# Kernel tuning notes

Measured on AMD Instinct MI355X. Metric: run time of the kernel, lower is better.

Reference implementation:

```python
import jax, jax.numpy as jnp
import numpy as np
import math

B, S, D, H = 2, 2048, 4096, 32
HD = D // H  # 128


def setup_inputs() -> dict:
    key = jax.random.key(0)
    ks = jax.random.split(key, 8)
    x = jax.random.normal(ks[0], (B, S, D), dtype=jnp.float32)
    wq = jax.random.normal(ks[1], (D, D), dtype=jnp.float32) * 0.02
    wk = jax.random.normal(ks[2], (D, D), dtype=jnp.float32) * 0.02
    wv = jax.random.normal(ks[3], (D, D), dtype=jnp.float32) * 0.02
    wo = jax.random.normal(ks[4], (D, D), dtype=jnp.float32) * 0.02
    # RoPE frequencies as in LLaMA: theta = 10000^{-2i/hd}
    inv_freq = 1.0 / (10000.0 ** (np.arange(0, HD, 2, dtype=np.float32) / HD))  # [HD/2]
    t = np.arange(S, dtype=np.float32)
    freqs = np.outer(t, inv_freq)  # [S, HD/2]
    freqs_cos = jnp.asarray(np.cos(freqs))
    freqs_sin = jnp.asarray(np.sin(freqs))
    # additive causal mask [1,1,S,S]
    neg = jnp.full((S, S), -1e9, dtype=jnp.float32)
    mask = jnp.triu(neg, k=1)[None, None, :, :]
    return {"x": x, "wq": wq, "wk": wk, "wv": wv, "wo": wo,
            "freqs_cos": freqs_cos, "freqs_sin": freqs_sin, "mask": mask}


def _apply_rope(t, cos, sin):
    # t: [b, s, h, hd]; cos/sin: [s, hd/2]. Complex mult on (even, odd) pairs.
    tr = t.reshape(*t.shape[:-1], HD // 2, 2)
    xr, xi = tr[..., 0], tr[..., 1]
    c = cos[None, :, None, :]
    s = sin[None, :, None, :]
    out_r = xr * c - xi * s
    out_i = xr * s + xi * c
    return jnp.stack([out_r, out_i], axis=-1).reshape(t.shape)


def reference(x, wq, wk, wv, wo, freqs_cos, freqs_sin, mask):
    b, s, d = x.shape
    # projections (nn.Linear: y = x @ W^T)
    xq = (x @ wq.T).reshape(b, s, H, HD)
    xk = (x @ wk.T).reshape(b, s, H, HD)
    xv = (x @ wv.T).reshape(b, s, H, HD)
    xq = _apply_rope(xq, freqs_cos, freqs_sin)
    xk = _apply_rope(xk, freqs_cos, freqs_sin)
    # [b,h,q,k] scores, softmax in fp32, then attend
    scores = jnp.einsum('bqhd,bkhd->bhqk', xq, xk) / math.sqrt(HD)
    scores = scores + mask
    probs = jax.nn.softmax(scores.astype(jnp.float32), axis=-1).astype(xq.dtype)
    out = jnp.einsum('bhqk,bkhd->bqhd', probs, xv).reshape(b, s, d)
    return out @ wo.T
```

## Files before the change

### kernel.cpp

```cpp
#include <hip/hip_runtime.h>

typedef __bf16 bf16x8 __attribute__((ext_vector_type(8)));
typedef float f32x4 __attribute__((ext_vector_type(4)));
typedef float f32x16 __attribute__((ext_vector_type(16)));
typedef unsigned short u16;
typedef unsigned int u32;
typedef u16 u16x8 __attribute__((ext_vector_type(8)));
typedef u16 u16x4 __attribute__((ext_vector_type(4)));
typedef u32 u32x4 __attribute__((ext_vector_type(4)));

#define B_ 2
#define S_ 2048
#define D_ 4096
#define H_ 32
#define HD_ 128
#define SM_SCALE 0.08838834764831845f
#define C2_ 0.12751743f

__device__ __forceinline__ u16 f2bf(float f) {
  __bf16 h = (__bf16)f;
  return __builtin_bit_cast(unsigned short, h);
}
__device__ __forceinline__ float bf2f(u16 u) {
  return (float)__builtin_bit_cast(__bf16, u);
}

#define GLD_TO_LDS16(gsrc, ldst)                                                     \
  __builtin_amdgcn_global_load_lds((__attribute__((address_space(1))) void*)(gsrc),  \
                                   (__attribute__((address_space(3))) void*)(ldst),  \
                                   16, 0, 0)

__global__ __launch_bounds__(256) void cvt_kernel(const float* __restrict__ src,
                                                  u16* __restrict__ dst, int n4) {
  int i = blockIdx.x * blockDim.x + threadIdx.x;
  int stride = gridDim.x * blockDim.x;
  for (; i < n4; i += stride) {
    float4 v = reinterpret_cast<const float4*>(src)[i];
    u16x4 o;
    o[0] = f2bf(v.x); o[1] = f2bf(v.y); o[2] = f2bf(v.z); o[3] = f2bf(v.w);
    reinterpret_cast<u16x4*>(dst)[i] = o;
  }
}

__global__ __launch_bounds__(256) void rope_kernel(u16* __restrict__ T,
                                                   const float* __restrict__ fc,
                                                   const float* __restrict__ fs) {
  const int n = B_ * S_ * D_ / 2;
  int i = blockIdx.x * blockDim.x + threadIdx.x;
  int stride = gridDim.x * blockDim.x;
  unsigned int* Tp = reinterpret_cast<unsigned int*>(T);
  for (; i < n; i += stride) {
    int row = i >> 11;
    int pr = i & 2047;
    int s = row & (S_ - 1);
    int p = pr & 63;
    float c = fc[(s << 6) + p];
    float sn = fs[(s << 6) + p];
    unsigned int u = Tp[i];
    float xr = bf2f((u16)(u & 0xffff));
    float xi = bf2f((u16)(u >> 16));
    float orr = xr * c - xi * sn;
    float oii = xr * sn + xi * c;
    Tp[i] = (unsigned int)f2bf(orr) | ((unsigned int)f2bf(oii) << 16);
  }
}


#define LGKM0()                                            \
  do {                                                     \
    asm volatile("s_waitcnt lgkmcnt(0)" ::: "memory");     \
    __builtin_amdgcn_sched_barrier(0);                     \
  } while (0)

__device__ __forceinline__ void fill_af(bf16x8 (&dst)[4], const u16* half_base,
                                        int wr, int lane, int ks) {
#pragma unroll
  for (int m = 0; m < 4; ++m) {
    int rr = wr * 64 + m * 16 + (lane & 15);
    int c8 = (ks * 4 + (lane >> 4)) ^ (rr & 7);
    dst[m] = *reinterpret_cast<const bf16x8*>(half_base + rr * 64 + c8 * 8);
  }
}
__device__ __forceinline__ void fill_bf(bf16x8 (&dst)[2][2], const u16* half_base,
                                        int wn, int lane) {
#pragma unroll
  for (int ks = 0; ks < 2; ++ks)
#pragma unroll
    for (int n = 0; n < 2; ++n) {
      int rr = wn * 32 + n * 16 + (lane & 15);
      int c8 = (ks * 4 + (lane >> 4)) ^ (rr & 7);
      dst[ks][n] = *reinterpret_cast<const bf16x8*>(half_base + rr * 64 + c8 * 8);
    }
}

#define MFMA8(MQ, NQ, KS, AF, BF)                                                \
  do {                                                                           \
    __builtin_amdgcn_s_setprio(1);                                               \
    _Pragma("unroll") for (int m = 0; m < 4; ++m)                                \
      _Pragma("unroll") for (int n = 0; n < 2; ++n)                              \
        acc[(MQ) * 4 + m][(NQ) * 2 + n] =                                        \
            __builtin_amdgcn_mfma_f32_16x16x32_bf16(                             \
                (AF)[m], (BF)[KS][n], acc[(MQ) * 4 + m][(NQ) * 2 + n], 0, 0, 0); \
    __builtin_amdgcn_s_setprio(0);                                               \
  } while (0)

template <typename OutT>
__global__ __launch_bounds__(512, 2) void gemm256_kernel(const u16* __restrict__ A,
                                                         const u16* __restrict__ Bw,
                                                         OutT* __restrict__ C,
                                                         int M, int N, int K) {
  __shared__ u16 As[2][2][8192];
  __shared__ u16 Bs[2][2][8192];
  const int tid = threadIdx.x;
  const int lane = tid & 63;
  const int w = tid >> 6;
  const int wr = w >> 2;
  const int wn = w & 3;
  const int nbx = N >> 8;
  const int nby = M >> 8;
  const int nwg = nby * nbx;
  int tr, tc;
  if (nby == 16 && nbx == 16) {
    int xcd = blockIdx.x & 7, j = blockIdx.x >> 3;
    tr = (xcd >> 1) * 4 + (j >> 3);
    tc = (xcd & 1) * 8 + (j & 7);
  } else {
    int wg = blockIdx.x;
    if ((nwg & 7) == 0) wg = (wg & 7) * (nwg >> 3) + (wg >> 3);
    tr = wg / nbx; tc = wg % nbx;
  }

  const size_t arow0 = (size_t)tr * 256;
  const size_t brow0 = (size_t)tc * 256;
  const int KT = K >> 6;

  auto stageA = [&](int t, int half) {
    if (t >= KT) return;
    const int k0 = t << 6;
    u16* base = &As[t & 1][half][0];
#pragma unroll
    for (int i = 0; i < 2; ++i) {
      int q = i * 512 + tid;
      int r = q >> 3;
      int c8 = (q & 7) ^ (r & 7);
      GLD_TO_LDS16(A + (arow0 + half * 128 + r) * K + k0 + c8 * 8, base + q * 8);
    }
  };
  auto stageB = [&](int t, int half) {
    if (t >= KT) return;
    const int k0 = t << 6;
    u16* base = &Bs[t & 1][half][0];
#pragma unroll
    for (int i = 0; i < 2; ++i) {
      int q = i * 512 + tid;
      int r = q >> 3;
      int c8 = (q & 7) ^ (r & 7);
      GLD_TO_LDS16(Bw + (brow0 + half * 128 + r) * K + k0 + c8 * 8, base + q * 8);
    }
  };

  f32x4 acc[8][4] = {};
  bf16x8 afX[4], afY[4], bf0[2][2], bf1[2][2];

  stageA(0, 0); stageA(0, 1); stageB(0, 0); stageB(0, 1);
  stageB(1, 0); stageB(1, 1); stageA(1, 1);
  asm volatile("s_waitcnt vmcnt(4)" ::: "memory");
  __builtin_amdgcn_s_barrier();
  __builtin_amdgcn_sched_barrier(0);
  fill_af(afX, &As[0][0][0], wr, lane, 0);
  fill_bf(bf0, &Bs[0][0][0], wn, lane);

  for (int k = 0; k < KT; ++k) {
    const int buf = k & 1, nb = buf ^ 1;
    const u16* A0 = &As[buf][0][0];
    const u16* A1 = &As[buf][1][0];
    const u16* B1L = &Bs[buf][1][0];
    const u16* A0n = &As[nb][0][0];
    const u16* B0n = &Bs[nb][0][0];

    LGKM0();
    fill_af(afY, A0, wr, lane, 1);
    fill_bf(bf1, B1L, wn, lane);
    stageA(k + 1, 0);
    MFMA8(0, 0, 0, afX, bf0);
    LGKM0();
    fill_af(afX, A1, wr, lane, 0);
    MFMA8(0, 0, 1, afY, bf0);
    __builtin_amdgcn_s_barrier();

    LGKM0();
    fill_af(afY, A1, wr, lane, 1);
    stageB(k + 2, 0);
    MFMA8(1, 0, 0, afX, bf0);
    LGKM0();
    fill_af(afX, A1, wr, lane, 0);
    MFMA8(1, 0, 1, afY, bf0);
    __builtin_amdgcn_s_barrier();

    LGKM0();
    fill_af(afY, A1, wr, lane, 1);
    stageB(k + 2, 1);
    MFMA8(1, 1, 0, afX, bf1);
    LGKM0();
    fill_af(afX, A0, wr, lane, 0);
    MFMA8(1, 1, 1, afY, bf1);
    __builtin_amdgcn_s_barrier();

    LGKM0();
    fill_af(afY, A0, wr, lane, 1);
    MFMA8(0, 1, 0, afX, bf1);
    LGKM0();
    stageA(k + 2, 1);
    if (k >= KT - 3) asm volatile("s_waitcnt vmcnt(0)" ::: "memory");
    else             asm volatile("s_waitcnt vmcnt(4)" ::: "memory");
    __builtin_amdgcn_s_barrier();
    __builtin_amdgcn_sched_barrier(0);
    if (k + 1 < KT) {
      fill_af(afX, A0n, wr, lane, 0);
      fill_bf(bf0, B0n, wn, lane);
    }
    MFMA8(0, 1, 1, afY, bf1);
    __builtin_amdgcn_s_barrier();
  }

#pragma unroll
  for (int mi = 0; mi < 8; ++mi) {
    const int mq = mi >> 2, m = mi & 3;
#pragma unroll
    for (int ni = 0; ni < 4; ++ni) {
      const int nq = ni >> 1, n = ni & 1;
#pragma unroll
      for (int r = 0; r < 4; ++r) {
        size_t row = arow0 + mq * 128 + wr * 64 + m * 16 + ((lane >> 4) << 2) + r;
        size_t col = (size_t)tc * 256 + nq * 128 + wn * 32 + n * 16 + (lane & 15);
        float v = acc[mi][ni][r];
        if constexpr (__is_same(OutT, float)) {
          C[row * N + col] = v;
        } else {
          C[row * N + col] = f2bf(v);
        }
      }
    }
  }
}

__global__ __launch_bounds__(256, 2) void attn_kernel(const u16* __restrict__ Q,
                                                      const u16* __restrict__ K,
                                                      const u16* __restrict__ V,
                                                      u16* __restrict__ O) {
  __shared__ u16 Ks[2][64 * 128];
  __shared__ u16 Vt[2][128 * 64];

  const int blk = blockIdx.x;
  const int qt = 15 - (blk >> 6);
  const int bh = blk & 63;
  const int b = bh >> 5, h = bh & 31;
  const int q0 = qt << 7;
  const int tid = threadIdx.x, lane = tid & 63, w = tid >> 6;
  const int wq0 = q0 + w * 32;
  const int l31 = lane & 31;
  const int hi = lane >> 5;
  const int qg = wq0 + l31;

  bf16x8 qf[8];
#pragma unroll
  for (int kb = 0; kb < 8; ++kb)
    qf[kb] = *reinterpret_cast<const bf16x8*>(Q + (size_t)(b * S_ + qg) * D_ + h * HD_ + kb * 16 + hi * 8);

  f32x16 oacc[4] = {};
  float mrun = -__builtin_inff(), lrun = 0.f;

  const int ntiles = 2 * qt + 2;
  u16x8 vreg[4];

  {
#pragma unroll
    for (int it = 0; it < 4; ++it) {
      int ff = it * 256 + tid;
      int row = ff >> 4, cc = ff & 15;
      int scc = cc ^ (row & 7);
      GLD_TO_LDS16(K + (size_t)(b * S_ + row) * D_ + h * HD_ + scc * 8, &Ks[0][ff << 3]);
    }
#pragma unroll
    for (int it = 0; it < 4; ++it) {
      int ff = it * 256 + tid;
      int r = ff & 63, dc = ff >> 6;
      vreg[it] = *reinterpret_cast<const u16x8*>(V + (size_t)(b * S_ + r) * D_ + h * HD_ + dc * 8);
    }
#pragma unroll
    for (int it = 0; it < 4; ++it) {
      int ff = it * 256 + tid;
      int r = ff & 63, dc = ff >> 6;
#pragma unroll
      for (int j = 0; j < 8; ++j) {
        int d = dc * 8 + j;
        Vt[0][(d << 6) + (((r >> 3) ^ (d & 7)) << 3) + (r & 7)] = vreg[it][j];
      }
    }
  }
  __syncthreads();

  for (int t = 0; t < ntiles; ++t) {
    const int cur = t & 1, nxt = cur ^ 1;
    const bool pre = (t + 1 < ntiles);
    if (pre) {
      const int kv1 = (t + 1) << 6;
#pragma unroll
      for (int it = 0; it < 4; ++it) {
        int ff = it * 256 + tid;
        int row = ff >> 4, cc = ff & 15;
        int scc = cc ^ (row & 7);
        GLD_TO_LDS16(K + (size_t)(b * S_ + kv1 + row) * D_ + h * HD_ + scc * 8, &Ks[nxt][ff << 3]);
      }
#pragma unroll
      for (int it = 0; it < 4; ++it) {
        int ff = it * 256 + tid;
        int r = ff & 63, dc = ff >> 6;
        vreg[it] = *reinterpret_cast<const u16x8*>(V + (size_t)(b * S_ + kv1 + r) * D_ + h * HD_ + dc * 8);
      }
    }

    const int kv0 = t << 6;
    if (kv0 <= wq0 + 31) {
      f32x16 st[2] = {};
      __builtin_amdgcn_s_setprio(1);
#pragma unroll
      for (int kvh = 0; kvh < 2; ++kvh) {
#pragma unroll
        for (int kb = 0; kb < 8; ++kb) {
          int row = kvh * 32 + l31;
          int cc = (2 * kb + hi) ^ (row & 7);
          bf16x8 kf = *reinterpret_cast<const bf16x8*>(&Ks[cur][(row << 7) + (cc << 3)]);
          st[kvh] = __builtin_amdgcn_mfma_f32_32x32x16_bf16(kf, qf[kb], st[kvh], 0, 0, 0);
        }
      }
      __builtin_amdgcn_s_setprio(0);

      if (kv0 + 63 > wq0) {
#pragma unroll
        for (int kvh = 0; kvh < 2; ++kvh)
#pragma unroll
          for (int r = 0; r < 16; ++r) {
            int kvg = kv0 + kvh * 32 + (r & 3) + 8 * (r >> 2) + 4 * hi;
            if (kvg > qg) st[kvh][r] = -1e30f;
          }
      }

      float vmax = -1e30f;
#pragma unroll
      for (int kvh = 0; kvh < 2; ++kvh)
#pragma unroll
        for (int r = 0; r < 16; ++r) vmax = fmaxf(vmax, st[kvh][r]);
      vmax = fmaxf(vmax, __shfl_xor(vmax, 32));
      float mnew = fmaxf(mrun, vmax);
      float sc = exp2f((mrun - mnew) * C2_);
      mrun = mnew;
      float psum = 0.f;
#pragma unroll
      for (int kvh = 0; kvh < 2; ++kvh)
#pragma unroll
        for (int r = 0; r < 16; ++r) {
          float p = exp2f((st[kvh][r] - mnew) * C2_);
          st[kvh][r] = p;
          psum += p;
        }
      psum += __shfl_xor(psum, 32);
      lrun = lrun * sc + psum;
#pragma unroll
      for (int db = 0; db < 4; ++db)
#pragma unroll
        for (int r = 0; r < 16; ++r) oacc[db][r] *= sc;

      __builtin_amdgcn_s_setprio(1);
#pragma unroll
      for (int h2 = 0; h2 < 2; ++h2)
#pragma unroll
        for (int s2 = 0; s2 < 2; ++s2) {
          const int rb = s2 * 8;
          u32 w0, w1, w2, w3;
          asm("v_cvt_pk_bf16_f32 %0, %1, %2" : "=v"(w0) : "v"(st[h2][rb + 0]), "v"(st[h2][rb + 1]));
          asm("v_cvt_pk_bf16_f32 %0, %1, %2" : "=v"(w1) : "v"(st[h2][rb + 2]), "v"(st[h2][rb + 3]));
          asm("v_cvt_pk_bf16_f32 %0, %1, %2" : "=v"(w2) : "v"(st[h2][rb + 4]), "v"(st[h2][rb + 5]));
          asm("v_cvt_pk_bf16_f32 %0, %1, %2" : "=v"(w3) : "v"(st[h2][rb + 6]), "v"(st[h2][rb + 7]));
          u32 sw0 = (u32)__shfl_xor((int)w0, 32);
          u32 sw1 = (u32)__shfl_xor((int)w1, 32);
          u32 sw2 = (u32)__shfl_xor((int)w2, 32);
          u32 sw3 = (u32)__shfl_xor((int)w3, 32);
          u32x4 fw;
          fw[0] = hi ? sw2 : w0;
          fw[1] = hi ? sw3 : w1;
          fw[2] = hi ? w2 : sw0;
          fw[3] = hi ? w3 : sw1;
          bf16x8 pfrag = __builtin_bit_cast(bf16x8, fw);
#pragma unroll
          for (int db = 0; db < 4; ++db) {
            int d = db * 32 + l31;
            int cc = (h2 * 4 + s2 * 2 + hi) ^ (d & 7);
            bf16x8 va = *reinterpret_cast<const bf16x8*>(&Vt[cur][(d << 6) + (cc << 3)]);
            oacc[db] = __builtin_amdgcn_mfma_f32_32x32x16_bf16(va, pfrag, oacc[db], 0, 0, 0);
          }
        }
      __builtin_amdgcn_s_setprio(0);
    }

    if (pre) {
#pragma unroll
      for (int it = 0; it < 4; ++it) {
        int ff = it * 256 + tid;
        int r = ff & 63, dc = ff >> 6;
#pragma unroll
        for (int j = 0; j < 8; ++j) {
          int d = dc * 8 + j;
          Vt[nxt][(d << 6) + (((r >> 3) ^ (d & 7)) << 3) + (r & 7)] = vreg[it][j];
        }
      }
    }
    __syncthreads();
  }

  const float rinv = 1.0f / lrun;
#pragma unroll
  for (int db = 0; db < 4; ++db)
#pragma unroll
    for (int g = 0; g < 4; ++g) {
      u16x4 o4;
#pragma unroll
      for (int j = 0; j < 4; ++j) o4[j] = f2bf(oacc[db][g * 4 + j] * rinv);
      int d = db * 32 + g * 8 + 4 * hi;
      *reinterpret_cast<u16x4*>(O + (size_t)(b * S_ + qg) * D_ + h * HD_ + d) = o4;
    }
}

extern "C" void kernel_launch(void* const* d_in, const int* in_sizes, int n_in,
                              void* d_out, int out_size, void* d_ws, size_t ws_size,
                              hipStream_t stream) {
  const float* x = (const float*)d_in[0];
  const float* wq = (const float*)d_in[1];
  const float* wk = (const float*)d_in[2];
  const float* wv = (const float*)d_in[3];
  const float* wo = (const float*)d_in[4];
  const float* fc = (const float*)d_in[5];
  const float* fs = (const float*)d_in[6];
  float* out = (float*)d_out;

  const size_t SLOT = (size_t)B_ * S_ * D_;
  u16* ws = (u16*)d_ws;
  u16* wqb = ws + 0 * SLOT;
  u16* wkb = ws + 1 * SLOT;
  u16* wvb = ws + 2 * SLOT;
  u16* wob = ws + 3 * SLOT;
  u16* xb  = ws + 4 * SLOT;
  u16* Qb  = ws + 5 * SLOT;
  u16* Kb  = ws + 6 * SLOT;
  u16* Vb  = ws + 7 * SLOT;
  u16* Ob  = xb;

  const int n4 = (int)(SLOT / 4);
  cvt_kernel<<<2048, 256, 0, stream>>>(x, xb, n4);
  cvt_kernel<<<2048, 256, 0, stream>>>(wq, wqb, n4);
  cvt_kernel<<<2048, 256, 0, stream>>>(wk, wkb, n4);
  cvt_kernel<<<2048, 256, 0, stream>>>(wv, wvb, n4);
  cvt_kernel<<<2048, 256, 0, stream>>>(wo, wob, n4);

  gemm256_kernel<u16><<<256, 512, 0, stream>>>(xb, wqb, Qb, B_ * S_, D_, D_);
  gemm256_kernel<u16><<<256, 512, 0, stream>>>(xb, wkb, Kb, B_ * S_, D_, D_);
  gemm256_kernel<u16><<<256, 512, 0, stream>>>(xb, wvb, Vb, B_ * S_, D_, D_);

  rope_kernel<<<2048, 256, 0, stream>>>(Qb, fc, fs);
  rope_kernel<<<2048, 256, 0, stream>>>(Kb, fc, fs);

  attn_kernel<<<1024, 256, 0, stream>>>(Qb, Kb, Vb, Ob);

  gemm256_kernel<float><<<256, 512, 0, stream>>>(Ob, wob, out, B_ * S_, D_, D_);
}
```

Baseline: 709.5 us.

## Fuse RoPE into QK GEMM epilogue, merge casts, add lazy softmax rescale

Merges the five fp32-to-bf16 conversion launches into one kernel that picks source and destination by block region. Removes the two standalone RoPE passes by applying the rotation in the Q/K GEMM epilogue, using a lane-pair shuffle and reading cos/sin per output element. The attention softmax now rescales the running max and output accumulator only when some lane's new max exceeds the old one by more than a threshold. This skips many multiplies but lets exponents grow up to about 2^8 before rescaling.

```diff
diff --git a/kernel.cpp b/kernel.cpp
--- a/kernel.cpp
+++ b/kernel.cpp
@@ -30,38 +30,29 @@
                                    (__attribute__((address_space(3))) void*)(ldst),  \
                                    16, 0, 0)
 
-__global__ __launch_bounds__(256) void cvt_kernel(const float* __restrict__ src,
-                                                  u16* __restrict__ dst, int n4) {
-  int i = blockIdx.x * blockDim.x + threadIdx.x;
-  int stride = gridDim.x * blockDim.x;
+__global__ __launch_bounds__(256) void cvt5_kernel(const float* __restrict__ s0,
+                                                   const float* __restrict__ s1,
+                                                   const float* __restrict__ s2,
+                                                   const float* __restrict__ s3,
+                                                   const float* __restrict__ s4,
+                                                   u16* __restrict__ d0,
+                                                   u16* __restrict__ d1,
+                                                   u16* __restrict__ d2,
+                                                   u16* __restrict__ d3,
+                                                   u16* __restrict__ d4,
+                                                   int n4) {
+  const int region = blockIdx.x >> 9;
+  const float* src = region == 0 ? s0 : region == 1 ? s1 : region == 2 ? s2
+                   : region == 3 ? s3 : s4;
+  u16* dst = region == 0 ? d0 : region == 1 ? d1 : region == 2 ? d2
+           : region == 3 ? d3 : d4;
+  int i = (blockIdx.x & 511) * 256 + threadIdx.x;
+  const int stride = 512 * 256;
   for (; i < n4; i += stride) {
     float4 v = reinterpret_cast<const float4*>(src)[i];
     u16x4 o;
     o[0] = f2bf(v.x); o[1] = f2bf(v.y); o[2] = f2bf(v.z); o[3] = f2bf(v.w);
     reinterpret_cast<u16x4*>(dst)[i] = o;
-  }
-}
-
-__global__ __launch_bounds__(256) void rope_kernel(u16* __restrict__ T,
-                                                   const float* __restrict__ fc,
-                                                   const float* __restrict__ fs) {
-  const int n = B_ * S_ * D_ / 2;
-  int i = blockIdx.x * blockDim.x + threadIdx.x;
-  int stride = gridDim.x * blockDim.x;
-  unsigned int* Tp = reinterpret_cast<unsigned int*>(T);
-  for (; i < n; i += stride) {
-    int row = i >> 11;
-    int pr = i & 2047;
-    int s = row & (S_ - 1);
-    int p = pr & 63;
-    float c = fc[(s << 6) + p];
-    float sn = fs[(s << 6) + p];
-    unsigned int u = Tp[i];
-    float xr = bf2f((u16)(u & 0xffff));
-    float xi = bf2f((u16)(u >> 16));
-    float orr = xr * c - xi * sn;
-    float oii = xr * sn + xi * c;
-    Tp[i] = (unsigned int)f2bf(orr) | ((unsigned int)f2bf(oii) << 16);
   }
 }
 
@@ -104,11 +95,13 @@
     __builtin_amdgcn_s_setprio(0);                                               \
   } while (0)
 
-template <typename OutT>
+template <typename OutT, bool ROPE>
 __global__ __launch_bounds__(512, 2) void gemm256_kernel(const u16* __restrict__ A,
                                                          const u16* __restrict__ Bw,
                                                          OutT* __restrict__ C,
-                                                         int M, int N, int K) {
+                                                         int M, int N, int K,
+                                                         const float* __restrict__ fc,
+                                                         const float* __restrict__ fs) {
   __shared__ u16 As[2][2][8192];
   __shared__ u16 Bs[2][2][8192];
   const int tid = threadIdx.x;
@@ -234,6 +227,14 @@
         size_t row = arow0 + mq * 128 + wr * 64 + m * 16 + ((lane >> 4) << 2) + r;
         size_t col = (size_t)tc * 256 + nq * 128 + wn * 32 + n * 16 + (lane & 15);
         float v = acc[mi][ni][r];
+        if constexpr (ROPE) {
+          float o = __shfl_xor(v, 1);
+          int s = (int)(row & (S_ - 1));
+          int p = (wn * 32 + n * 16 + (lane & 14)) >> 1;
+          float cv = fc[(s << 6) + p];
+          float sv = fs[(s << 6) + p];
+          v = (lane & 1) ? (v * cv + o * sv) : (v * cv - o * sv);
+        }
         if constexpr (__is_same(OutT, float)) {
           C[row * N + col] = v;
         } else {
@@ -352,24 +353,27 @@
 #pragma unroll
         for (int r = 0; r < 16; ++r) vmax = fmaxf(vmax, st[kvh][r]);
       vmax = fmaxf(vmax, __shfl_xor(vmax, 32));
-      float mnew = fmaxf(mrun, vmax);
-      float sc = exp2f((mrun - mnew) * C2_);
-      mrun = mnew;
+      if (!__all(vmax <= mrun + 64.0f)) {
+        float mnew = fmaxf(mrun, vmax);
+        float sc = exp2f((mrun - mnew) * C2_);
+        mrun = mnew;
+        lrun *= sc;
+#pragma unroll
+        for (int db = 0; db < 4; ++db)
+#pragma unroll
+          for (int r = 0; r < 16; ++r) oacc[db][r] *= sc;
+      }
       float psum = 0.f;
 #pragma unroll
       for (int kvh = 0; kvh < 2; ++kvh)
 #pragma unroll
         for (int r = 0; r < 16; ++r) {
-          float p = exp2f((st[kvh][r] - mnew) * C2_);
+          float p = exp2f((st[kvh][r] - mrun) * C2_);
           st[kvh][r] = p;
           psum += p;
         }
       psum += __shfl_xor(psum, 32);
-      lrun = lrun * sc + psum;
-#pragma unroll
-      for (int db = 0; db < 4; ++db)
-#pragma unroll
-        for (int r = 0; r < 16; ++r) oacc[db][r] *= sc;
+      lrun += psum;
 
       __builtin_amdgcn_s_setprio(1);
 #pragma unroll
@@ -456,20 +460,13 @@
   u16* Ob  = xb;
 
   const int n4 = (int)(SLOT / 4);
-  cvt_kernel<<<2048, 256, 0, stream>>>(x, xb, n4);
-  cvt_kernel<<<2048, 256, 0, stream>>>(wq, wqb, n4);
-  cvt_kernel<<<2048, 256, 0, stream>>>(wk, wkb, n4);
-  cvt_kernel<<<2048, 256, 0, stream>>>(wv, wvb, n4);
-  cvt_kernel<<<2048, 256, 0, stream>>>(wo, wob, n4);
-
-  gemm256_kernel<u16><<<256, 512, 0, stream>>>(xb, wqb, Qb, B_ * S_, D_, D_);
-  gemm256_kernel<u16><<<256, 512, 0, stream>>>(xb, wkb, Kb, B_ * S_, D_, D_);
-  gemm256_kernel<u16><<<256, 512, 0, stream>>>(xb, wvb, Vb, B_ * S_, D_, D_);
-
-  rope_kernel<<<2048, 256, 0, stream>>>(Qb, fc, fs);
-  rope_kernel<<<2048, 256, 0, stream>>>(Kb, fc, fs);
+  cvt5_kernel<<<2560, 256, 0, stream>>>(x, wq, wk, wv, wo, xb, wqb, wkb, wvb, wob, n4);
+
+  gemm256_kernel<u16, true><<<256, 512, 0, stream>>>(xb, wqb, Qb, B_ * S_, D_, D_, fc, fs);
+  gemm256_kernel<u16, true><<<256, 512, 0, stream>>>(xb, wkb, Kb, B_ * S_, D_, D_, fc, fs);
+  gemm256_kernel<u16, false><<<256, 512, 0, stream>>>(xb, wvb, Vb, B_ * S_, D_, D_, fc, fs);
 
   attn_kernel<<<1024, 256, 0, stream>>>(Qb, Kb, Vb, Ob);
 
-  gemm256_kernel<float><<<256, 512, 0, stream>>>(Ob, wob, out, B_ * S_, D_, D_);
-}
+  gemm256_kernel<float, false><<<256, 512, 0, stream>>>(Ob, wob, out, B_ * S_, D_, D_, fc, fs);
+}
```

Measured after the change: 680.4 us. 4.1% less time.
